# Optimization experiments

Measured on AMD Instinct MI355X. Metric: run time of the kernel, lower is better.

The kernel has to match this reference:

```python
import jax, jax.numpy as jnp
import numpy as np

B, S, D = 8, 1024, 1024      # batch, seq_len, inp_dim
H, HD = 8, 64                # head_num, head_dim
HID = H * HD                 # hidden_dim = 512
P = 2 * D                    # p_factor * inp_dim = 2048
K = 4                        # causal conv kernel size
EPS = 1e-6
CAP = 15.0                   # soft cap for i/f gates


def _layernorm(x, g, b):
    mu = jnp.mean(x, -1, keepdims=True)
    var = jnp.var(x, -1, keepdims=True)
    return (x - mu) * jax.lax.rsqrt(var + EPS) * g + b


def _soft_cap(v):
    return CAP * jnp.tanh(v / CAP)


def _causal_conv_feat(x, w, b):
    # Conv1d(1,1,K) applied over the FEATURE axis of each timestep (as in the
    # torch code: x_t.unsqueeze(1) -> (bs,1,P)), causal left pad of K-1.
    L = x.shape[-1]
    xp = jnp.pad(x, ((0, 0), (0, 0), (K - 1, 0)))
    out = b
    for m in range(K):
        out = out + w[m] * xp[..., m:m + L]
    return out


def _forward(x, ln_g, ln_b, mh_g, mh_b, W_up_l, b_up_l, W_up_r, b_up_r,
             W_down, b_down, conv_w, conv_b, W_skip, b_skip, W_i, b_i,
             W_f, b_f, W_o, b_o, W_q, b_q, W_k, b_k, W_v, b_v):
    Bs, Sl, _ = x.shape
    xn = _layernorm(x, ln_g, ln_b)
    x_t = xn @ W_up_l.T + b_up_l                      # (B,S,P)
    r_t = xn @ W_up_r.T + b_up_r                      # (B,S,HID)
    x_c = jax.nn.silu(_causal_conv_feat(x_t, conv_w, conv_b))
    x_skip = x_c @ W_skip.T + b_skip                  # (B,S,HID)
    q = (x_c @ W_q.T + b_q).reshape(Bs, Sl, H, HD)
    k = (x_c @ W_k.T + b_k).reshape(Bs, Sl, H, HD) / float(np.sqrt(HD))
    v = (x_t @ W_v.T + b_v).reshape(Bs, Sl, H, HD)
    i_pre = _soft_cap(x_c @ W_i.T + b_i)              # (B,S,H)
    f_pre = _soft_cap(x_c @ W_f.T + b_f)              # (B,S,H)
    o = jax.nn.sigmoid(x_t @ W_o.T + b_o)             # (B,S,HID)

    def step(carry, inp):
        c, n, m = carry
        qt, kt, vt, it, ft = inp
        m_t = jnp.maximum(ft + m, it)
        ie = jnp.exp(it - m_t)
        fe = jnp.exp(ft - m_t + m)
        c = fe[:, :, None, None] * c + ie[:, :, None, None] * jnp.einsum('bhd,bhe->bhde', vt, kt)
        n = fe[:, :, None] * n + ie[:, :, None] * kt
        num = jnp.einsum('bhde,bhe->bhd', c, qt)
        den = jnp.maximum(jnp.sum(n * qt, -1, keepdims=True), 1.0)
        return (c, n, m_t), num / den

    c0 = jnp.zeros((Bs, H, HD, HD), x.dtype)
    n0 = jnp.ones((Bs, H, HD), x.dtype)
    m0 = jnp.zeros((Bs, H), x.dtype)
    seq = tuple(jnp.moveaxis(a, 1, 0) for a in (q, k, v, i_pre, f_pre))
    _, hs = jax.lax.scan(step, (c0, n0, m0), seq)     # hs: (S,B,H,HD)
    h = o * jnp.moveaxis(hs, 0, 1).reshape(Bs, Sl, HID)
    hn = _layernorm(h.reshape(Bs, Sl, H, HD), mh_g, mh_b).reshape(Bs, Sl, HID)
    out = (hn + x_skip) * jax.nn.silu(r_t)
    return out @ W_down.T + b_down + x


def setup_inputs() -> dict:
    key = jax.random.key(0)
    ks = jax.random.split(key, 16)

    def w(kk, shape):
        return jax.random.normal(kk, shape, jnp.float32) / np.sqrt(shape[-1]).astype(np.float32)

    return {
        'x': jax.random.normal(ks[0], (B, S, D), jnp.float32),
        'ln_g': jnp.ones((D,), jnp.float32), 'ln_b': jnp.zeros((D,), jnp.float32),
        'mh_g': jnp.ones((H, HD), jnp.float32), 'mh_b': jnp.zeros((H, HD), jnp.float32),
        'W_up_l': w(ks[1], (P, D)), 'b_up_l': jnp.zeros((P,), jnp.float32),
        'W_up_r': w(ks[2], (HID, D)), 'b_up_r': jnp.zeros((HID,), jnp.float32),
        'W_down': w(ks[3], (D, HID)), 'b_down': jnp.zeros((D,), jnp.float32),
        'conv_w': jax.random.normal(ks[4], (K,), jnp.float32) * 0.3,
        'conv_b': jnp.zeros((), jnp.float32),
        'W_skip': w(ks[5], (HID, P)), 'b_skip': jnp.zeros((HID,), jnp.float32),
        'W_i': w(ks[6], (H, P)), 'b_i': jnp.zeros((H,), jnp.float32),
        'W_f': w(ks[7], (H, P)), 'b_f': jnp.zeros((H,), jnp.float32),
        'W_o': w(ks[8], (HID, P)), 'b_o': jnp.zeros((HID,), jnp.float32),
        'W_q': w(ks[9], (HID, P)), 'b_q': jnp.zeros((HID,), jnp.float32),
        'W_k': w(ks[10], (HID, P)), 'b_k': jnp.zeros((HID,), jnp.float32),
        'W_v': w(ks[11], (HID, P)), 'b_v': jnp.zeros((HID,), jnp.float32),
    }


def reference(x, ln_g, ln_b, mh_g, mh_b, W_up_l, b_up_l, W_up_r, b_up_r,
              W_down, b_down, conv_w, conv_b, W_skip, b_skip, W_i, b_i,
              W_f, b_f, W_o, b_o, W_q, b_q, W_k, b_k, W_v, b_v):
    return _forward(x, ln_g, ln_b, mh_g, mh_b, W_up_l, b_up_l, W_up_r, b_up_r,
                    W_down, b_down, conv_w, conv_b, W_skip, b_skip, W_i, b_i,
                    W_f, b_f, W_o, b_o, W_q, b_q, W_k, b_k, W_v, b_v)
```

## Files before the change

### kernel.cpp

```cpp
#include <hip/hip_runtime.h>
#include <hip/hip_bf16.h>
#include <math.h>

#define Bq 8
#define Sq 1024
#define Dq 1024
#define Hq 8
#define HDq 64
#define HIDq 512
#define Pq 2048
#define EPSq 1e-6f
#define CAPq 15.0f
#define NCq 16
#define CLq 64
#define LDST 40
#define ARENA (128 * LDST)
#define GEMM_SMEM_BYTES (2 * 4 * ARENA * 2)

typedef __attribute__((ext_vector_type(8))) short short8;
typedef __attribute__((ext_vector_type(4))) float f32x4v;
typedef __hip_bfloat16 bf16;

__device__ inline void split2(float v, bf16& h, bf16& l) {
  h = __float2bfloat16(v);
  l = __float2bfloat16(v - __bfloat162float(h));
}

__device__ inline float bfs2f(short s) {
  bf16 t = *(const bf16*)&s;
  return __bfloat162float(t);
}

__global__ __launch_bounds__(256) void cvtw_all(
    const float* __restrict__ s0, const float* __restrict__ s1,
    const float* __restrict__ s2, const float* __restrict__ s3,
    const float* __restrict__ s4, const float* __restrict__ s5,
    const float* __restrict__ s6, const float* __restrict__ s7,
    bf16* __restrict__ hi, bf16* __restrict__ lo)
{
  int u = blockIdx.x * 256 + threadIdx.x;
  const float* src; int segBase;
  if      (u <  524288) { src = s0; segBase = 0;       }
  else if (u <  655360) { src = s1; segBase = 524288;  }
  else if (u <  917504) { src = s2; segBase = 655360;  }
  else if (u < 1179648) { src = s3; segBase = 917504;  }
  else if (u < 1441792) { src = s4; segBase = 1179648; }
  else if (u < 1703936) { src = s5; segBase = 1441792; }
  else if (u < 1966080) { src = s6; segBase = 1703936; }
  else                  { src = s7; segBase = 1966080; }
  float4 v = ((const float4*)src)[u - segBase];
  size_t o = (size_t)u * 4;
  bf16 h, l;
  split2(v.x, h, l); hi[o+0] = h; lo[o+0] = l;
  split2(v.y, h, l); hi[o+1] = h; lo[o+1] = l;
  split2(v.z, h, l); hi[o+2] = h; lo[o+2] = l;
  split2(v.w, h, l); hi[o+3] = h; lo[o+3] = l;
}

__global__ __launch_bounds__(256) void ln_kernel(const float* __restrict__ x,
    const float* __restrict__ g, const float* __restrict__ b,
    bf16* __restrict__ yh, bf16* __restrict__ yl)
{
  int row = blockIdx.x;
  int tid = threadIdx.x;
  const float* xr = x + (size_t)row * Dq;
  float v[4]; float s = 0.f, s2 = 0.f;
  #pragma unroll
  for (int i = 0; i < 4; i++) { v[i] = xr[tid + 256*i]; s += v[i]; s2 += v[i]*v[i]; }
  #pragma unroll
  for (int mm = 32; mm > 0; mm >>= 1) { s += __shfl_xor(s, mm, 64); s2 += __shfl_xor(s2, mm, 64); }
  __shared__ float rs[4], rs2[4];
  int lane = tid & 63, wave = tid >> 6;
  if (lane == 0) { rs[wave] = s; rs2[wave] = s2; }
  __syncthreads();
  s  = rs[0] + rs[1] + rs[2] + rs[3];
  s2 = rs2[0] + rs2[1] + rs2[2] + rs2[3];
  float mu  = s * (1.f / Dq);
  float var = s2 * (1.f / Dq) - mu * mu;
  float r = rsqrtf(var + EPSq);
  #pragma unroll
  for (int i = 0; i < 4; i++) {
    int c = tid + 256*i;
    float y = (v[i] - mu) * r * g[c] + b[c];
    bf16 h, l; split2(y, h, l);
    yh[(size_t)row * Dq + c] = h;
    yl[(size_t)row * Dq + c] = l;
  }
}

__global__ __launch_bounds__(256) void gemm_x3(
    const bf16* __restrict__ Ahi, const bf16* __restrict__ Alo,
    const bf16* __restrict__ Whi, const bf16* __restrict__ Wlo,
    int Kd, int start1, int start2, const float* __restrict__ resid,
    const float* bias0, float* f0, bf16* h0, bf16* l0, int w0, float sc0, int a0,
    const float* bias1, float* f1, bf16* h1, bf16* l1, int w1, float sc1, int a1,
    const float* bias2, float* f2, bf16* h2, bf16* l2, int w2, float sc2, int a2)
{
  extern __shared__ short smem[];
  int tid = threadIdx.x;
  int lane = tid & 63, wave = tid >> 6;
  int wr = wave >> 1, wc = wave & 1;

  int gx = gridDim.x;
  int flat = blockIdx.y * gx + blockIdx.x;
  int nb = gx * gridDim.y;
  int chunk = nb >> 3;
  int nid = (flat & 7) * chunk + (flat >> 3);
  int col = nid % gx, row = nid / gx;
  int rowBase = row * 128;
  int colBase = col * 128;

  int sk  = (tid & 3) * 8;
  int sr0 = tid >> 2;
  int sr1 = 64 + sr0;

  const short* Ahg = (const short*)Ahi + (size_t)rowBase * Kd;
  const short* Alg = (const short*)Alo + (size_t)rowBase * Kd;
  const short* Bhg = (const short*)Whi + (size_t)colBase * Kd;
  const short* Blg = (const short*)Wlo + (size_t)colBase * Kd;

  f32x4v acc[4][4];
  #pragma unroll
  for (int i = 0; i < 4; i++)
    #pragma unroll
    for (int j = 0; j < 4; j++) acc[i][j] = (f32x4v){0.f, 0.f, 0.f, 0.f};

  int fk = (lane >> 4) * 8;
  int fr = lane & 15;
  int nk = Kd >> 5;

  short8 ah0, ah1, al0, al1, bh0, bh1, bl0, bl1;

#define LOAD_TILE(k0) do {                                                    \
    size_t o0 = (size_t)sr0 * Kd + (k0) + sk;                                 \
    size_t o1 = (size_t)sr1 * Kd + (k0) + sk;                                 \
    ah0 = *(const short8*)(Ahg + o0); ah1 = *(const short8*)(Ahg + o1);       \
    al0 = *(const short8*)(Alg + o0); al1 = *(const short8*)(Alg + o1);       \
    bh0 = *(const short8*)(Bhg + o0); bh1 = *(const short8*)(Bhg + o1);       \
    bl0 = *(const short8*)(Blg + o0); bl1 = *(const short8*)(Blg + o1);       \
  } while (0)

#define STORE_TILE(S) do {                                                    \
    *(short8*)&(S)[0*ARENA + sr0*LDST + sk] = ah0;                            \
    *(short8*)&(S)[0*ARENA + sr1*LDST + sk] = ah1;                            \
    *(short8*)&(S)[1*ARENA + sr0*LDST + sk] = al0;                            \
    *(short8*)&(S)[1*ARENA + sr1*LDST + sk] = al1;                            \
    *(short8*)&(S)[2*ARENA + sr0*LDST + sk] = bh0;                            \
    *(short8*)&(S)[2*ARENA + sr1*LDST + sk] = bh1;                            \
    *(short8*)&(S)[3*ARENA + sr0*LDST + sk] = bl0;                            \
    *(short8*)&(S)[3*ARENA + sr1*LDST + sk] = bl1;                            \
  } while (0)

  LOAD_TILE(0);
  STORE_TILE(smem);
  __syncthreads();

  for (int t = 0; t < nk; ++t) {
    const short* C = smem + (t & 1) * (4 * ARENA);
    short* Nx      = smem + ((t + 1) & 1) * (4 * ARENA);
    bool pf = (t + 1 < nk);
    if (pf) LOAD_TILE((size_t)(t + 1) << 5);

    short8 afh[4], afl[4], bfh[4], bfl[4];
    #pragma unroll
    for (int mi = 0; mi < 4; mi++) {
      afh[mi] = *(const short8*)&C[0*ARENA + (wr * 64 + mi * 16 + fr) * LDST + fk];
      afl[mi] = *(const short8*)&C[1*ARENA + (wr * 64 + mi * 16 + fr) * LDST + fk];
    }
    #pragma unroll
    for (int ni = 0; ni < 4; ni++) {
      bfh[ni] = *(const short8*)&C[2*ARENA + (wc * 64 + ni * 16 + fr) * LDST + fk];
      bfl[ni] = *(const short8*)&C[3*ARENA + (wc * 64 + ni * 16 + fr) * LDST + fk];
    }
    #pragma unroll
    for (int mi = 0; mi < 4; mi++)
      #pragma unroll
      for (int ni = 0; ni < 4; ni++)
        acc[mi][ni] = __builtin_amdgcn_mfma_f32_16x16x32_bf16(afh[mi], bfh[ni], acc[mi][ni], 0, 0, 0);
    #pragma unroll
    for (int mi = 0; mi < 4; mi++)
      #pragma unroll
      for (int ni = 0; ni < 4; ni++)
        acc[mi][ni] = __builtin_amdgcn_mfma_f32_16x16x32_bf16(afh[mi], bfl[ni], acc[mi][ni], 0, 0, 0);
    #pragma unroll
    for (int mi = 0; mi < 4; mi++)
      #pragma unroll
      for (int ni = 0; ni < 4; ni++)
        acc[mi][ni] = __builtin_amdgcn_mfma_f32_16x16x32_bf16(afl[mi], bfh[ni], acc[mi][ni], 0, 0, 0);

    __builtin_amdgcn_sched_barrier(0);
    if (pf) STORE_TILE(Nx);
    __syncthreads();
  }
#undef LOAD_TILE
#undef STORE_TILE

  const float* bias; float* fOut; bf16* hOut; bf16* lOut; int segStart, segW; float sscale; int sact;
  if (colBase >= start2)      { bias=bias2; fOut=f2; hOut=h2; lOut=l2; segStart=start2; segW=w2; sscale=sc2; sact=a2; }
  else if (colBase >= start1) { bias=bias1; fOut=f1; hOut=h1; lOut=l1; segStart=start1; segW=w1; sscale=sc1; sact=a1; }
  else                        { bias=bias0; fOut=f0; hOut=h0; lOut=l0; segStart=0;      segW=w0; sscale=sc0; sact=a0; }

  int cr = (lane >> 4) * 4;
  int cc = lane & 15;
  #pragma unroll
  for (int mi = 0; mi < 4; mi++) {
    #pragma unroll
    for (int ni = 0; ni < 4; ni++) {
      int colO  = colBase + wc * 64 + ni * 16 + cc;
      int colL = colO - segStart;
      float bv = bias[colL];
      #pragma unroll
      for (int j = 0; j < 4; j++) {
        int rowO = rowBase + wr * 64 + mi * 16 + cr + j;
        float val = (acc[mi][ni][j] + bv) * sscale;
        if (sact) val = 1.f / (1.f + expf(-val));
        if (resid && segStart == 0) val += resid[(size_t)rowO * segW + colL];
        size_t oidx = (size_t)rowO * segW + colL;
        if (fOut) fOut[oidx] = val;
        if (hOut) {
          bf16 h, l; split2(val, h, l);
          hOut[oidx] = h; lOut[oidx] = l;
        }
      }
    }
  }
}

__global__ __launch_bounds__(256) void conv_kernel(const bf16* __restrict__ xth,
    const bf16* __restrict__ xtl, const float* __restrict__ cw,
    const float* __restrict__ cb, bf16* __restrict__ xch, bf16* __restrict__ xcl,
    int total8)
{
  int u = blockIdx.x * 256 + threadIdx.x;
  if (u >= total8) return;
  size_t idx = (size_t)u * 8;
  int p0 = (int)(idx & (Pq - 1));
  const short* hp = (const short*)xth + idx;
  const short* lp = (const short*)xtl + idx;
  short8 ch = *(const short8*)hp;
  short8 cl = *(const short8*)lp;
  float xv[11];
  #pragma unroll
  for (int j = 0; j < 8; j++) xv[3 + j] = bfs2f(ch[j]) + bfs2f(cl[j]);
  if (p0 > 0) {
    short8 ph = *(const short8*)(hp - 8);
    short8 pl = *(const short8*)(lp - 8);
    xv[0] = bfs2f(ph[5]) + bfs2f(pl[5]);
    xv[1] = bfs2f(ph[6]) + bfs2f(pl[6]);
    xv[2] = bfs2f(ph[7]) + bfs2f(pl[7]);
  } else {
    xv[0] = xv[1] = xv[2] = 0.f;
  }
  float w0 = cw[0], w1 = cw[1], w2 = cw[2], w3 = cw[3], bb = cb[0];
  short8 oh, ol;
  #pragma unroll
  for (int j = 0; j < 8; j++) {
    float acc = bb + w3 * xv[j + 3] + w2 * xv[j + 2] + w1 * xv[j + 1] + w0 * xv[j];
    float y = acc / (1.f + expf(-acc));
    bf16 h, l; split2(y, h, l);
    oh[j] = *(const short*)&h;
    ol[j] = *(const short*)&l;
  }
  *(short8*)((short*)xch + idx) = oh;
  *(short8*)((short*)xcl + idx) = ol;
}

__global__ __launch_bounds__(256) void ifk_kernel(const bf16* __restrict__ xch,
    const bf16* __restrict__ xcl,
    const float* __restrict__ Wi, const float* __restrict__ bi,
    const float* __restrict__ Wf, const float* __restrict__ bf_,
    float* __restrict__ ip, float* __restrict__ fp)
{
  int row = blockIdx.x;
  int lane = threadIdx.x & 63, wave = threadIdx.x >> 6;
  size_t rb = (size_t)row * Pq;
  const short* xh = (const short*)xch + rb;
  const short* xl = (const short*)xcl + rb;
  for (int oi = wave; oi < 16; oi += 4) {
    int hh = oi & 7;
    const float* Wrow = (oi < 8) ? (Wi + (size_t)hh * Pq) : (Wf + (size_t)hh * Pq);
    float s = 0.f;
    for (int j0 = lane * 8; j0 < Pq; j0 += 512) {
      short8 hv = *(const short8*)(xh + j0);
      short8 lv = *(const short8*)(xl + j0);
      float4 wa = *(const float4*)(Wrow + j0);
      float4 wb = *(const float4*)(Wrow + j0 + 4);
      s += (bfs2f(hv[0]) + bfs2f(lv[0])) * wa.x;
      s += (bfs2f(hv[1]) + bfs2f(lv[1])) * wa.y;
      s += (bfs2f(hv[2]) + bfs2f(lv[2])) * wa.z;
      s += (bfs2f(hv[3]) + bfs2f(lv[3])) * wa.w;
      s += (bfs2f(hv[4]) + bfs2f(lv[4])) * wb.x;
      s += (bfs2f(hv[5]) + bfs2f(lv[5])) * wb.y;
      s += (bfs2f(hv[6]) + bfs2f(lv[6])) * wb.z;
      s += (bfs2f(hv[7]) + bfs2f(lv[7])) * wb.w;
    }
    #pragma unroll
    for (int mm = 32; mm > 0; mm >>= 1) s += __shfl_xor(s, mm, 64);
    if (lane == 0) {
      float val = s + ((oi < 8) ? bi[hh] : bf_[hh]);
      val = CAPq * tanhf(val / CAPq);
      if (oi < 8) ip[(size_t)row * Hq + hh] = val;
      else        fp[(size_t)row * Hq + hh] = val;
    }
  }
}

__global__ __launch_bounds__(256) void chunkA_kernel(const float* __restrict__ k,
    const float* __restrict__ v, const float* __restrict__ ip,
    const float* __restrict__ fp, float* __restrict__ bg,
    float* __restrict__ FcMc, float* __restrict__ kvg, float* __restrict__ ksumg)
{
  int blk = blockIdx.x;
  int bh = blk >> 4, c = blk & 15;
  int b = bh >> 3, hh = bh & 7;
  int tid = threadIdx.x, lane = tid & 63, wave = tid >> 6;

  __shared__ float sK[64][64], sV[64][64], sW[64];

  size_t base = (size_t)b * Sq * 512 + (size_t)hh * 64 + (size_t)c * CLq * 512;
  #pragma unroll 4
  for (int i = 0; i < 16; i++) {
    int t = wave * 16 + i;
    sK[t][lane] = k[base + (size_t)t * 512 + lane];
    sV[t][lane] = v[base + (size_t)t * 512 + lane];
  }
  if (tid < 64) {
    size_t ifb = ((size_t)b * Sq + c * CLq + tid) * Hq + hh;
    float fv = fp[ifb], iv = ip[ifb];
    float cf = fv;
    #pragma unroll
    for (int off = 1; off < 64; off <<= 1) {
      float t2 = __shfl_up(cf, off, 64);
      if (lane >= off) cf += t2;
    }
    float bs = iv - cf;
    float mx = bs;
    #pragma unroll
    for (int off = 1; off < 64; off <<= 1) {
      float t2 = __shfl_up(mx, off, 64);
      if (lane >= off) mx = fmaxf(mx, t2);
    }
    float Mc = __shfl(mx, 63, 64);
    bg[(size_t)blk * 64 + tid] = bs;
    sW[tid] = expf(bs - Mc);
    if (tid == 63) { FcMc[blk*2] = cf; FcMc[blk*2+1] = Mc; }
  }
  __syncthreads();
  float acc[16];
  #pragma unroll
  for (int j = 0; j < 16; j++) acc[j] = 0.f;
  for (int s = 0; s < 64; s++) {
    float wv = sW[s] * sV[s][lane];
    #pragma unroll
    for (int j = 0; j < 16; j++) acc[j] += wv * sK[s][wave*16+j];
  }
  float* kvp = kvg + (size_t)blk * 4096 + lane * 64 + wave * 16;
  #pragma unroll
  for (int j = 0; j < 16; j++) kvp[j] = acc[j];
  if (tid < 64) {
    float a = 0.f;
    for (int s = 0; s < 64; s++) a += sW[s] * sK[s][tid];
    ksumg[(size_t)blk * 64 + tid] = a;
  }
}

__global__ __launch_bounds__(256) void chunkB_kernel(const float* __restrict__ kvg,
    const float* __restrict__ ksumg, const float* __restrict__ FcMc,
    float* __restrict__ boundC, float* __restrict__ boundN, float* __restrict__ boundM)
{
  int bh = blockIdx.x;
  int tid = threadIdx.x, lane = tid & 63, wave = tid >> 6;
  float C[16];
  #pragma unroll
  for (int j = 0; j < 16; j++) C[j] = 0.f;
  float ne = 1.0f, m = 0.f;
  for (int c = 0; c < NCq; c++) {
    size_t blk = (size_t)bh * NCq + c;
    float* bC = boundC + blk * 4096 + lane * 64 + wave * 16;
    #pragma unroll
    for (int j = 0; j < 16; j++) bC[j] = C[j];
    if (wave == 0) boundN[blk * 64 + lane] = ne;
    if (tid == 0)  boundM[blk] = m;
    float Fc = FcMc[blk * 2], Mc = FcMc[blk * 2 + 1];
    float mm = fmaxf(m, Mc);
    float a1 = expf(m - mm), a2 = expf(Mc - mm);
    const float* kv = kvg + blk * 4096 + lane * 64 + wave * 16;
    #pragma unroll
    for (int j = 0; j < 16; j++) C[j] = a1 * C[j] + a2 * kv[j];
    ne = a1 * ne + a2 * ksumg[blk * 64 + lane];
    m = Fc + mm;
  }
}

__global__ __launch_bounds__(256) void chunkC_kernel(const float* q,
    const float* __restrict__ k, const float* __restrict__ v,
    const float* __restrict__ bg, const float* __restrict__ boundC,
    const float* __restrict__ boundN, const float* __restrict__ boundM,
    float* hs)
{
  int blk = blockIdx.x;
  int bh = blk >> 4, c = blk & 15;
  int b = bh >> 3, hh = bh & 7;
  int tid = threadIdx.x, lane = tid & 63, wave = tid >> 6;

  __shared__ float sQ[64][65], sKV[64][65], sS[64][65];
  __shared__ float sB[64], sMr[64], sNin[64];

  size_t base = (size_t)b * Sq * 512 + (size_t)hh * 64 + (size_t)c * CLq * 512;
  #pragma unroll 4
  for (int i = 0; i < 16; i++) {
    int t = wave * 16 + i;
    sQ[t][lane]  = q[base + (size_t)t * 512 + lane];
    sKV[t][lane] = k[base + (size_t)t * 512 + lane];
  }
  float m_in = boundM[blk];
  if (tid < 64) {
    float bs = bg[(size_t)blk * 64 + tid];
    float mx = bs;
    #pragma unroll
    for (int off = 1; off < 64; off <<= 1) {
      float t2 = __shfl_up(mx, off, 64);
      if (lane >= off) mx = fmaxf(mx, t2);
    }
    sB[tid]   = bs;
    sMr[tid]  = fmaxf(m_in, mx);
    sNin[tid] = boundN[(size_t)blk * 64 + tid];
  }
  __syncthreads();

  {
    int t = lane;
    float acc[16];
    #pragma unroll
    for (int j = 0; j < 16; j++) acc[j] = 0.f;
    for (int d = 0; d < 64; d++) {
      float qv = sQ[t][d];
      #pragma unroll
      for (int j = 0; j < 16; j++) acc[j] += qv * sKV[wave*16+j][d];
    }
    float Mr = sMr[t];
    #pragma unroll
    for (int j = 0; j < 16; j++) {
      int s = wave * 16 + j;
      float w = (s <= t) ? expf(sB[s] - Mr) : 0.f;
      sS[t][s] = w * acc[j];
    }
  }
  __syncthreads();
  #pragma unroll 4
  for (int i = 0; i < 16; i++) {
    int t = wave * 16 + i;
    sKV[t][lane] = v[base + (size_t)t * 512 + lane];
  }
  __syncthreads();

  {
    int t = lane;
    float Mr = sMr[t];
    float bfac = expf(m_in - Mr);
    float den = 0.f;
    for (int d = 0; d < 64; d++) den += sNin[d] * sQ[t][d];
    den *= bfac;
    float num[16];
    #pragma unroll
    for (int j = 0; j < 16; j++) num[j] = 0.f;
    const float* Crow = boundC + (size_t)blk * 4096;
    for (int e = 0; e < 64; e++) {
      float qv = sQ[t][e];
      #pragma unroll
      for (int j = 0; j < 16; j++)
        num[j] += Crow[(size_t)(wave*16+j) * 64 + e] * qv;
    }
    #pragma unroll
    for (int j = 0; j < 16; j++) num[j] *= bfac;
    for (int s = 0; s < 64; s++) {
      float ws = sS[t][s];
      den += ws;
      #pragma unroll
      for (int j = 0; j < 16; j++) num[j] += ws * sKV[s][wave*16+j];
    }
    den = fmaxf(den, 1.0f);
    float o[16];
    #pragma unroll
    for (int j = 0; j < 16; j++) o[j] = num[j] / den;
    float* hp = hs + base + (size_t)t * 512 + wave * 16;
    #pragma unroll
    for (int j4 = 0; j4 < 4; j4++)
      ((float4*)hp)[j4] = ((float4*)o)[j4];
  }
}

__global__ __launch_bounds__(256) void epi_kernel(const float* __restrict__ hsv,
    const float* __restrict__ ov, const float* __restrict__ xs,
    const float* __restrict__ rt, const float* __restrict__ mg,
    const float* __restrict__ mb, bf16* __restrict__ pdh, bf16* __restrict__ pdl)
{
  int tid = threadIdx.x;
  int lane = tid & 63, wave = tid >> 6;
  size_t row = (size_t)blockIdx.x * 4 + wave;
  int hh = (int)(row & 7);
  size_t idx = row * 64 + lane;
  float hv = ov[idx] * hsv[idx];
  float s = hv, s2 = hv * hv;
  #pragma unroll
  for (int mm = 32; mm > 0; mm >>= 1) { s += __shfl_xor(s, mm, 64); s2 += __shfl_xor(s2, mm, 64); }
  float mu  = s * (1.f / 64.f);
  float var = s2 * (1.f / 64.f) - mu * mu;
  float r = rsqrtf(var + EPSq);
  float hn = (hv - mu) * r * mg[hh * 64 + lane] + mb[hh * 64 + lane];
  float rv = rt[idx];
  float y = (hn + xs[idx]) * (rv / (1.f + expf(-rv)));
  bf16 h, l; split2(y, h, l);
  pdh[idx] = h; pdl[idx] = l;
}

extern "C" void kernel_launch(void* const* d_in, const int* in_sizes, int n_in,
                              void* d_out, int out_size, void* d_ws, size_t ws_size,
                              hipStream_t stream)
{
  const float* x      = (const float*)d_in[0];
  const float* ln_g   = (const float*)d_in[1];
  const float* ln_b   = (const float*)d_in[2];
  const float* mh_g   = (const float*)d_in[3];
  const float* mh_b   = (const float*)d_in[4];
  const float* W_up_l = (const float*)d_in[5];
  const float* b_up_l = (const float*)d_in[6];
  const float* W_up_r = (const float*)d_in[7];
  const float* b_up_r = (const float*)d_in[8];
  const float* W_down = (const float*)d_in[9];
  const float* b_down = (const float*)d_in[10];
  const float* conv_w = (const float*)d_in[11];
  const float* conv_b = (const float*)d_in[12];
  const float* W_skip = (const float*)d_in[13];
  const float* b_skip = (const float*)d_in[14];
  const float* W_i    = (const float*)d_in[15];
  const float* b_i    = (const float*)d_in[16];
  const float* W_f    = (const float*)d_in[17];
  const float* b_f    = (const float*)d_in[18];
  const float* W_o    = (const float*)d_in[19];
  const float* b_o    = (const float*)d_in[20];
  const float* W_q    = (const float*)d_in[21];
  const float* b_q    = (const float*)d_in[22];
  const float* W_k    = (const float*)d_in[23];
  const float* b_k    = (const float*)d_in[24];
  const float* W_v    = (const float*)d_in[25];
  const float* b_v    = (const float*)d_in[26];
  float* out = (float*)d_out;

  const size_t MB = 1u << 20;
  if (ws_size < 193 * MB) return;

  static bool attrSet = false;
  if (!attrSet) {
    (void)hipFuncSetAttribute(reinterpret_cast<const void*>(gemm_x3),
                              hipFuncAttributeMaxDynamicSharedMemorySize,
                              GEMM_SMEM_BYTES);
    attrSet = true;
  }

  char* base = (char*)d_ws;
  bf16* whi = (bf16*)base;
  bf16* wlo = (bf16*)(base + 16*MB);
  bf16* xnh = (bf16*)(base + 32*MB);
  bf16* xnl = (bf16*)(base + 48*MB);
  bf16* xth = (bf16*)(base + 64*MB);
  bf16* xtl = (bf16*)(base + 96*MB);
  bf16* xch = (bf16*)(base + 128*MB);
  bf16* xcl = (bf16*)(base + 160*MB);
  float* vb  = (float*)(base + 32*MB);
  float* ob  = (float*)(base + 48*MB);
  float* xs  = (float*)(base + 64*MB);
  float* qb  = (float*)(base + 80*MB);
  float* kb  = (float*)(base + 96*MB);
  bf16*  pdh = (bf16*)(base + 112*MB);
  bf16*  pdl = (bf16*)(base + 120*MB);
  float* kvg    = (float*)(base + 128*MB);
  float* boundC = (float*)(base + 144*MB);
  float* bg     = (float*)(base + 160*MB);
  float* ksumg  = (float*)(base + 160*MB + 256*1024);
  float* boundN = (float*)(base + 160*MB + 512*1024);
  float* FcMc   = (float*)(base + 160*MB + 768*1024);
  float* boundM = (float*)(base + 160*MB + 776*1024);
  float* ip  = (float*)(base + 192*MB);
  float* fpb = (float*)(base + 192*MB + 256*1024);
  float* rt  = out;
  float* hsb = qb;

  const int Mrows = Bq * Sq;
  const int BIG = 1 << 30;

  cvtw_all<<<dim3(8192), dim3(256), 0, stream>>>(
      W_up_l, W_up_r, W_v, W_o, W_skip, W_q, W_k, W_down, whi, wlo);

  ln_kernel<<<dim3(Mrows), dim3(256), 0, stream>>>(x, ln_g, ln_b, xnh, xnl);

  gemm_x3<<<dim3(20, 64), dim3(256), GEMM_SMEM_BYTES, stream>>>(
      xnh, xnl, whi, wlo, 1024, 2048, BIG, nullptr,
      b_up_l, nullptr, xth, xtl, 2048, 1.f, 0,
      b_up_r, rt, nullptr, nullptr, 512, 1.f, 0,
      nullptr, nullptr, nullptr, nullptr, 1, 1.f, 0);

  gemm_x3<<<dim3(8, 64), dim3(256), GEMM_SMEM_BYTES, stream>>>(
      xth, xtl, whi + 2621440, wlo + 2621440, 2048, 512, BIG, nullptr,
      b_v, vb, nullptr, nullptr, 512, 1.f, 0,
      b_o, ob, nullptr, nullptr, 512, 1.f, 1,
      nullptr, nullptr, nullptr, nullptr, 1, 1.f, 0);

  int convTotal8 = Mrows * Pq / 8;
  conv_kernel<<<dim3(convTotal8 / 256), dim3(256), 0, stream>>>(
      xth, xtl, conv_w, conv_b, xch, xcl, convTotal8);

  gemm_x3<<<dim3(12, 64), dim3(256), GEMM_SMEM_BYTES, stream>>>(
      xch, xcl, whi + 4718592, wlo + 4718592, 2048, 512, 1024, nullptr,
      b_skip, xs, nullptr, nullptr, 512, 1.f, 0,
      b_q, qb, nullptr, nullptr, 512, 1.f, 0,
      b_k, kb, nullptr, nullptr, 512, 0.125f, 0);

  ifk_kernel<<<dim3(Mrows), dim3(256), 0, stream>>>(
      xch, xcl, W_i, b_i, W_f, b_f, ip, fpb);

  chunkA_kernel<<<dim3(Bq * Hq * NCq), dim3(256), 0, stream>>>(
      kb, vb, ip, fpb, bg, FcMc, kvg, ksumg);
  chunkB_kernel<<<dim3(Bq * Hq), dim3(256), 0, stream>>>(
      kvg, ksumg, FcMc, boundC, boundN, boundM);
  chunkC_kernel<<<dim3(Bq * Hq * NCq), dim3(256), 0, stream>>>(
      qb, kb, vb, bg, boundC, boundN, boundM, hsb);

  epi_kernel<<<dim3(Mrows * Hq / 4), dim3(256), 0, stream>>>(
      hsb, ob, xs, rt, mh_g, mh_b, pdh, pdl);

  gemm_x3<<<dim3(8, 64), dim3(256), GEMM_SMEM_BYTES, stream>>>(
      pdh, pdl, whi + 7864320, wlo + 7864320, 512, BIG, BIG, x,
      b_down, out, nullptr, nullptr, 1024, 1.f, 0,
      nullptr, nullptr, nullptr, nullptr, 1, 1.f, 0,
      nullptr, nullptr, nullptr, nullptr, 1, 1.f, 0);
}
```

Baseline: 905.3 us.

## Deepen GEMM prefetch pipeline and vectorize chunk kernel loads

The GEMM main loop now prefetches two tiles ahead: it writes the next tile to shared memory before the MFMAs, issues the global load for the tile after that, raises wave priority during the MFMA block, and replaces __syncthreads with an explicit waitcnt plus s_barrier. The chunk kernels switch their global loads to float4 vectors, and chunkB runs 1024 threads with one float4 each instead of 256 threads with 16 scalars. The aim is to hide global-load latency behind matrix math in the dominant GEMMs and to cut per-thread serial work in the chunk scan. In exchange, the GEMM holds more registers for in-flight loads and depends on hand-placed barriers being correct.

```diff
diff --git a/kernel.cpp b/kernel.cpp
--- a/kernel.cpp
+++ b/kernel.cpp
@@ -153,13 +153,13 @@
 
   LOAD_TILE(0);
   STORE_TILE(smem);
-  __syncthreads();
+  if (nk > 1) LOAD_TILE(32);
+  asm volatile("s_waitcnt lgkmcnt(0)" ::: "memory");
+  __builtin_amdgcn_s_barrier();
 
   for (int t = 0; t < nk; ++t) {
     const short* C = smem + (t & 1) * (4 * ARENA);
     short* Nx      = smem + ((t + 1) & 1) * (4 * ARENA);
-    bool pf = (t + 1 < nk);
-    if (pf) LOAD_TILE((size_t)(t + 1) << 5);
 
     short8 afh[4], afl[4], bfh[4], bfl[4];
     #pragma unroll
@@ -172,6 +172,12 @@
       bfh[ni] = *(const short8*)&C[2*ARENA + (wc * 64 + ni * 16 + fr) * LDST + fk];
       bfl[ni] = *(const short8*)&C[3*ARENA + (wc * 64 + ni * 16 + fr) * LDST + fk];
     }
+    __builtin_amdgcn_sched_barrier(0);
+    if (t + 1 < nk) STORE_TILE(Nx);
+    __builtin_amdgcn_sched_barrier(0);
+    if (t + 2 < nk) LOAD_TILE((size_t)(t + 2) << 5);
+    __builtin_amdgcn_sched_barrier(0);
+    __builtin_amdgcn_s_setprio(1);
     #pragma unroll
     for (int mi = 0; mi < 4; mi++)
       #pragma unroll
@@ -187,10 +193,10 @@
       #pragma unroll
       for (int ni = 0; ni < 4; ni++)
         acc[mi][ni] = __builtin_amdgcn_mfma_f32_16x16x32_bf16(afl[mi], bfh[ni], acc[mi][ni], 0, 0, 0);
-
+    __builtin_amdgcn_s_setprio(0);
+    asm volatile("s_waitcnt lgkmcnt(0)" ::: "memory");
     __builtin_amdgcn_sched_barrier(0);
-    if (pf) STORE_TILE(Nx);
-    __syncthreads();
+    __builtin_amdgcn_s_barrier();
   }
 #undef LOAD_TILE
 #undef STORE_TILE
@@ -318,11 +324,12 @@
   __shared__ float sK[64][64], sV[64][64], sW[64];
 
   size_t base = (size_t)b * Sq * 512 + (size_t)hh * 64 + (size_t)c * CLq * 512;
-  #pragma unroll 4
-  for (int i = 0; i < 16; i++) {
-    int t = wave * 16 + i;
-    sK[t][lane] = k[base + (size_t)t * 512 + lane];
-    sV[t][lane] = v[base + (size_t)t * 512 + lane];
+  int tr = tid >> 4, c4 = (tid & 15) * 4;
+  #pragma unroll
+  for (int p = 0; p < 4; p++) {
+    int t = p * 16 + tr;
+    *(float4*)&sK[t][c4] = *(const float4*)(k + base + (size_t)t * 512 + c4);
+    *(float4*)&sV[t][c4] = *(const float4*)(v + base + (size_t)t * 512 + c4);
   }
   if (tid < 64) {
     size_t ifb = ((size_t)b * Sq + c * CLq + tid) * Hq + hh;
@@ -364,30 +371,30 @@
   }
 }
 
-__global__ __launch_bounds__(256) void chunkB_kernel(const float* __restrict__ kvg,
+__global__ __launch_bounds__(1024) void chunkB_kernel(const float* __restrict__ kvg,
     const float* __restrict__ ksumg, const float* __restrict__ FcMc,
     float* __restrict__ boundC, float* __restrict__ boundN, float* __restrict__ boundM)
 {
   int bh = blockIdx.x;
-  int tid = threadIdx.x, lane = tid & 63, wave = tid >> 6;
-  float C[16];
-  #pragma unroll
-  for (int j = 0; j < 16; j++) C[j] = 0.f;
+  int tid = threadIdx.x;
+  int r  = tid >> 4;
+  int cq = (tid & 15) * 4;
+  float4 C4 = {0.f, 0.f, 0.f, 0.f};
   float ne = 1.0f, m = 0.f;
   for (int c = 0; c < NCq; c++) {
     size_t blk = (size_t)bh * NCq + c;
-    float* bC = boundC + blk * 4096 + lane * 64 + wave * 16;
-    #pragma unroll
-    for (int j = 0; j < 16; j++) bC[j] = C[j];
-    if (wave == 0) boundN[blk * 64 + lane] = ne;
-    if (tid == 0)  boundM[blk] = m;
+    *(float4*)(boundC + blk * 4096 + r * 64 + cq) = C4;
+    if ((tid & 15) == 0) boundN[blk * 64 + r] = ne;
+    if (tid == 0)        boundM[blk] = m;
     float Fc = FcMc[blk * 2], Mc = FcMc[blk * 2 + 1];
     float mm = fmaxf(m, Mc);
     float a1 = expf(m - mm), a2 = expf(Mc - mm);
-    const float* kv = kvg + blk * 4096 + lane * 64 + wave * 16;
-    #pragma unroll
-    for (int j = 0; j < 16; j++) C[j] = a1 * C[j] + a2 * kv[j];
-    ne = a1 * ne + a2 * ksumg[blk * 64 + lane];
+    float4 kv = *(const float4*)(kvg + blk * 4096 + r * 64 + cq);
+    C4.x = a1 * C4.x + a2 * kv.x;
+    C4.y = a1 * C4.y + a2 * kv.y;
+    C4.z = a1 * C4.z + a2 * kv.z;
+    C4.w = a1 * C4.w + a2 * kv.w;
+    ne = a1 * ne + a2 * ksumg[blk * 64 + r];
     m = Fc + mm;
   }
 }
@@ -407,11 +414,14 @@
   __shared__ float sB[64], sMr[64], sNin[64];
 
   size_t base = (size_t)b * Sq * 512 + (size_t)hh * 64 + (size_t)c * CLq * 512;
-  #pragma unroll 4
-  for (int i = 0; i < 16; i++) {
-    int t = wave * 16 + i;
-    sQ[t][lane]  = q[base + (size_t)t * 512 + lane];
-    sKV[t][lane] = k[base + (size_t)t * 512 + lane];
+  int tr = tid >> 4, c4 = (tid & 15) * 4;
+  #pragma unroll
+  for (int p = 0; p < 4; p++) {
+    int t = p * 16 + tr;
+    float4 qv = *(const float4*)(q + base + (size_t)t * 512 + c4);
+    float4 kv = *(const float4*)(k + base + (size_t)t * 512 + c4);
+    sQ[t][c4+0] = qv.x; sQ[t][c4+1] = qv.y; sQ[t][c4+2] = qv.z; sQ[t][c4+3] = qv.w;
+    sKV[t][c4+0] = kv.x; sKV[t][c4+1] = kv.y; sKV[t][c4+2] = kv.z; sKV[t][c4+3] = kv.w;
   }
   float m_in = boundM[blk];
   if (tid < 64) {
@@ -447,10 +457,11 @@
     }
   }
   __syncthreads();
-  #pragma unroll 4
-  for (int i = 0; i < 16; i++) {
-    int t = wave * 16 + i;
-    sKV[t][lane] = v[base + (size_t)t * 512 + lane];
+  #pragma unroll
+  for (int p = 0; p < 4; p++) {
+    int t = p * 16 + tr;
+    float4 vv = *(const float4*)(v + base + (size_t)t * 512 + c4);
+    sKV[t][c4+0] = vv.x; sKV[t][c4+1] = vv.y; sKV[t][c4+2] = vv.z; sKV[t][c4+3] = vv.w;
   }
   __syncthreads();
 
@@ -621,7 +632,7 @@
 
   chunkA_kernel<<<dim3(Bq * Hq * NCq), dim3(256), 0, stream>>>(
       kb, vb, ip, fpb, bg, FcMc, kvg, ksumg);
-  chunkB_kernel<<<dim3(Bq * Hq), dim3(256), 0, stream>>>(
+  chunkB_kernel<<<dim3(Bq * Hq), dim3(1024), 0, stream>>>(
       kvg, ksumg, FcMc, boundC, boundN, boundM);
   chunkC_kernel<<<dim3(Bq * Hq * NCq), dim3(256), 0, stream>>>(
       qb, kb, vb, bg, boundC, boundN, boundM, hsb);
```

Measured after the change: 866.2 us. -4.3%, faster.
